# Performance work log

Measured on AMD Instinct MI355X. Metric: run time of the kernel, lower is better.

The kernel has to match this reference:

```python
import jax, jax.numpy as jnp
import numpy as np

B, H, W, C = 8, 128, 128, 64


def setup_inputs() -> dict:
    key = jax.random.key(0)
    x = jax.random.normal(key, (B, H, W, C), dtype=jnp.float32)
    return {"x": x}


def reference(x):
    # Criss-cross affinity: for each pixel (i,j), dot products against
    # the rest of its row (order: k<j then k>j) followed by its full column.
    b, h, w, c = x.shape
    # Row affinities: [B,H,W,W], A_row[b,i,j,k] = <x[b,i,j], x[b,i,k]>
    a_row = jnp.einsum('bijc,bikc->bijk', x, x)
    # Column affinities: [B,H,W,H], A_col[b,i,j,m] = <x[b,i,j], x[b,m,j]>
    a_col = jnp.einsum('bijc,bmjc->bijm', x, x)
    # Remove the self entry k=j from row affinities, preserving order
    # [0..j-1, j+1..W-1] to match the original tf.concat.
    idx = np.array([[k for k in range(w) if k != j] for j in range(w)],
                   dtype=np.int32)  # [W, W-1]
    row_part = jnp.take_along_axis(a_row, jnp.asarray(idx)[None, None, :, :],
                                   axis=3)  # [B,H,W,W-1]
    # Output: [B, H, W, (W-1)+H]
    return jnp.concatenate([row_part, a_col], axis=-1)
```

## Files before the change

kernel.cpp:

```cpp
#include <hip/hip_runtime.h>
#include <stdint.h>

#define BB 8
#define HH 128
#define WW 128
#define CC 64
#define OUTW 255

#define LDS_STRIDE 72
#define EP_STRIDE 130

typedef __attribute__((ext_vector_type(8))) short bf16x8;
typedef __attribute__((ext_vector_type(4))) float f32x4;

__device__ __forceinline__ unsigned short f2bf(float f) {
    union { float f; uint32_t u; } v; v.f = f;
    uint32_t u = v.u;
    return (unsigned short)((u + 0x7FFFu + ((u >> 16) & 1u)) >> 16);
}

__global__ __launch_bounds__(256)
void criss_cross_gram_kernel(const float* __restrict__ x, float* __restrict__ out) {
    __shared__ unsigned short xs[128 * LDS_STRIDE];
    __shared__ float ep[4][16 * EP_STRIDE];

    const int g = blockIdx.x;
    const int b = g >> 8;
    const int rem = g & 255;
    const bool isCol = (rem & 1);
    const int p = rem >> 1;

    const float* xbase;
    int xRowStride;
    int outBase;
    int outRowStride;
    if (!isCol) {
        xbase        = x + ((b * HH + p) * WW) * CC;
        xRowStride   = CC;
        outBase      = ((b * HH + p) * WW) * OUTW;
        outRowStride = OUTW;
    } else {
        xbase        = x + (b * HH * WW + p) * CC;
        xRowStride   = WW * CC;
        outBase      = (b * HH * WW + p) * OUTW;
        outRowStride = WW * OUTW;
    }

    const int t = threadIdx.x;

    #pragma unroll
    for (int r = 0; r < 8; ++r) {
        const int idx = r * 256 + t;
        const int row = idx >> 4;
        const int c4  = (idx & 15) << 2;
        const float4 v = *(const float4*)(xbase + row * xRowStride + c4);
        ushort4* dst = (ushort4*)&xs[row * LDS_STRIDE + c4];
        *dst = make_ushort4(f2bf(v.x), f2bf(v.y), f2bf(v.z), f2bf(v.w));
    }
    __syncthreads();

    const int wave = t >> 6;
    const int lane = t & 63;
    const int m16  = lane & 15;
    const int quad = lane >> 4;

    f32x4 acc[2][8];
    #pragma unroll
    for (int rt = 0; rt < 2; ++rt)
        #pragma unroll
        for (int ct = 0; ct < 8; ++ct)
            acc[rt][ct] = (f32x4){0.f, 0.f, 0.f, 0.f};

    #pragma unroll
    for (int ks = 0; ks < 2; ++ks) {
        const int kOff = ks * 32 + quad * 8;
        bf16x8 afrag[2];
        #pragma unroll
        for (int rt = 0; rt < 2; ++rt) {
            const int row = wave * 32 + rt * 16 + m16;
            afrag[rt] = *(const bf16x8*)&xs[row * LDS_STRIDE + kOff];
        }
        #pragma unroll
        for (int ct = 0; ct < 8; ++ct) {
            const int row = ct * 16 + m16;
            const bf16x8 bfrag = *(const bf16x8*)&xs[row * LDS_STRIDE + kOff];
            acc[0][ct] = __builtin_amdgcn_mfma_f32_16x16x32_bf16(afrag[0], bfrag, acc[0][ct], 0, 0, 0);
            acc[1][ct] = __builtin_amdgcn_mfma_f32_16x16x32_bf16(afrag[1], bfrag, acc[1][ct], 0, 0, 0);
        }
    }

    float* myep = &ep[wave][0];

    #pragma unroll
    for (int rt = 0; rt < 2; ++rt) {
        const int rowBase = wave * 32 + rt * 16;

        #pragma unroll
        for (int ct = 0; ct < 8; ++ct) {
            #pragma unroll
            for (int reg = 0; reg < 4; ++reg) {
                const int rl = quad * 4 + reg;
                const int gm = rowBase + rl;
                const int gn = ct * 16 + m16;
                const float v = acc[rt][ct][reg];
                if (isCol) {
                    myep[rl * EP_STRIDE + gn] = v;
                } else if (gn != gm) {
                    myep[rl * EP_STRIDE + (gn - (gn > gm ? 1 : 0))] = v;
                }
            }
        }

        #pragma unroll
        for (int r = 0; r < 16; ++r) {
            float* rp = out + outBase + (rowBase + r) * outRowStride + (isCol ? 127 : 0);
            rp[lane] = myep[r * EP_STRIDE + lane];
            if (isCol || lane < 63)
                rp[64 + lane] = myep[r * EP_STRIDE + 64 + lane];
        }
    }
}

extern "C" void kernel_launch(void* const* d_in, const int* in_sizes, int n_in,
                              void* d_out, int out_size, void* d_ws, size_t ws_size,
                              hipStream_t stream) {
    const float* x = (const float*)d_in[0];
    float* out = (float*)d_out;
    criss_cross_gram_kernel<<<dim3(BB * (HH + WW)), dim3(256), 0, stream>>>(x, out);
}
```

Baseline: 163.9 us.

## Alias epilogue staging onto input LDS and prefetch loads into registers

Reuses the bf16 input LDS buffer for the epilogue staging, splitting each 16-row tile into two 8-row passes so the staging fits. This shrinks total LDS per block, and launch bounds now request 4 blocks per SM. Global loads are issued into registers before the accumulator init and bf16 conversion so their latency overlaps. The cost is an extra barrier and more register pressure from holding eight float4 values, and the EP stride changes to 132.

```diff
diff --git a/kernel.cpp b/kernel.cpp
--- a/kernel.cpp
+++ b/kernel.cpp
@@ -8,7 +8,7 @@
 #define OUTW 255
 
 #define LDS_STRIDE 72
-#define EP_STRIDE 130
+#define EP_STRIDE 132
 
 typedef __attribute__((ext_vector_type(8))) short bf16x8;
 typedef __attribute__((ext_vector_type(4))) float f32x4;
@@ -19,10 +19,10 @@
     return (unsigned short)((u + 0x7FFFu + ((u >> 16) & 1u)) >> 16);
 }
 
-__global__ __launch_bounds__(256)
+__global__ __launch_bounds__(256, 4)
 void criss_cross_gram_kernel(const float* __restrict__ x, float* __restrict__ out) {
-    __shared__ unsigned short xs[128 * LDS_STRIDE];
-    __shared__ float ep[4][16 * EP_STRIDE];
+    __shared__ __align__(16) unsigned char smem[128 * LDS_STRIDE * 2];
+    unsigned short* xs = (unsigned short*)smem;
 
     const int g = blockIdx.x;
     const int b = g >> 8;
@@ -47,22 +47,19 @@
     }
 
     const int t = threadIdx.x;
+    const int wave = t >> 6;
+    const int lane = t & 63;
+    const int m16  = lane & 15;
+    const int quad = lane >> 4;
 
+    float4 v[8];
     #pragma unroll
     for (int r = 0; r < 8; ++r) {
         const int idx = r * 256 + t;
         const int row = idx >> 4;
         const int c4  = (idx & 15) << 2;
-        const float4 v = *(const float4*)(xbase + row * xRowStride + c4);
-        ushort4* dst = (ushort4*)&xs[row * LDS_STRIDE + c4];
-        *dst = make_ushort4(f2bf(v.x), f2bf(v.y), f2bf(v.z), f2bf(v.w));
+        v[r] = *(const float4*)(xbase + row * xRowStride + c4);
     }
-    __syncthreads();
-
-    const int wave = t >> 6;
-    const int lane = t & 63;
-    const int m16  = lane & 15;
-    const int quad = lane >> 4;
 
     f32x4 acc[2][8];
     #pragma unroll
@@ -70,6 +67,16 @@
         #pragma unroll
         for (int ct = 0; ct < 8; ++ct)
             acc[rt][ct] = (f32x4){0.f, 0.f, 0.f, 0.f};
+
+    #pragma unroll
+    for (int r = 0; r < 8; ++r) {
+        const int idx = r * 256 + t;
+        const int row = idx >> 4;
+        const int c4  = (idx & 15) << 2;
+        ushort4* dst = (ushort4*)&xs[row * LDS_STRIDE + c4];
+        *dst = make_ushort4(f2bf(v[r].x), f2bf(v[r].y), f2bf(v[r].z), f2bf(v[r].w));
+    }
+    __syncthreads();
 
     #pragma unroll
     for (int ks = 0; ks < 2; ++ks) {
@@ -89,34 +96,41 @@
         }
     }
 
-    float* myep = &ep[wave][0];
+    __syncthreads();
+
+    float* myep = (float*)smem + wave * (8 * EP_STRIDE);
 
     #pragma unroll
     for (int rt = 0; rt < 2; ++rt) {
         const int rowBase = wave * 32 + rt * 16;
 
         #pragma unroll
-        for (int ct = 0; ct < 8; ++ct) {
+        for (int c = 0; c < 2; ++c) {
             #pragma unroll
-            for (int reg = 0; reg < 4; ++reg) {
-                const int rl = quad * 4 + reg;
-                const int gm = rowBase + rl;
-                const int gn = ct * 16 + m16;
-                const float v = acc[rt][ct][reg];
-                if (isCol) {
-                    myep[rl * EP_STRIDE + gn] = v;
-                } else if (gn != gm) {
-                    myep[rl * EP_STRIDE + (gn - (gn > gm ? 1 : 0))] = v;
+            for (int ct = 0; ct < 8; ++ct) {
+                #pragma unroll
+                for (int rr = 0; rr < 2; ++rr) {
+                    const int reg  = 2 * c + rr;
+                    const int slot = quad * 2 + rr;
+                    const int gm   = rowBase + quad * 4 + reg;
+                    const int gn   = ct * 16 + m16;
+                    const float val = acc[rt][ct][reg];
+                    if (isCol) {
+                        myep[slot * EP_STRIDE + gn] = val;
+                    } else if (gn != gm) {
+                        myep[slot * EP_STRIDE + (gn - (gn > gm ? 1 : 0))] = val;
+                    }
                 }
             }
-        }
 
-        #pragma unroll
-        for (int r = 0; r < 16; ++r) {
-            float* rp = out + outBase + (rowBase + r) * outRowStride + (isCol ? 127 : 0);
-            rp[lane] = myep[r * EP_STRIDE + lane];
-            if (isCol || lane < 63)
-                rp[64 + lane] = myep[r * EP_STRIDE + 64 + lane];
+            #pragma unroll
+            for (int s = 0; s < 8; ++s) {
+                const int grow = rowBase + (s >> 1) * 4 + 2 * c + (s & 1);
+                float* rp = out + outBase + grow * outRowStride + (isCol ? 127 : 0);
+                rp[lane] = myep[s * EP_STRIDE + lane];
+                if (isCol || lane < 63)
+                    rp[64 + lane] = myep[s * EP_STRIDE + 64 + lane];
+            }
         }
     }
 }
```

Measured after the change: 165.1 us. Within noise of the previous version (+0.7%).
